# Performance work log

Hardware: AMD Instinct MI355X
Metric: run time of the kernel (lower is better)

The kernel has to match this reference:

```python
import jax, jax.numpy as jnp
import numpy as np

B, S, NC, ND, V = 16, 512, 10000, 10000, 128


def _rn(k, shape, scale=0.05):
    return jax.random.normal(k, shape, dtype=jnp.float32) * scale


def setup_inputs() -> dict:
    key = jax.random.key(0)
    ks = jax.random.split(key, 24)
    inp = {
        'c_seq': jax.random.randint(ks[0], (B, S), 0, NC),
        'd_seq': jax.random.randint(ks[1], (B, S), 0, ND),
        'r_seq': jax.random.uniform(ks[2], (B, S), dtype=jnp.float32),
        # embeddings / vectors
        'D1_w': _rn(ks[3], (ND, 1)),
        'D2_w': _rn(ks[4], (ND, V)),
        'v_r': _rn(ks[5], (V,)),
        'v_beta': _rn(ks[6], (V,)),
        # GRU (torch layout: gates ordered r,z,n; W_ih [3V,2V], W_hh [3V,V])
        'W_ih': _rn(ks[7], (3 * V, 2 * V)),
        'W_hh': _rn(ks[8], (3 * V, V)),
        'b_ih': jnp.zeros((3 * V,), jnp.float32),
        'b_hh': jnp.zeros((3 * V,), jnp.float32),
        # linear_1: V -> V -> V -> 1 (weights stored [in, out])
        'm1_W1': _rn(ks[9], (V, V)), 'm1_b1': jnp.zeros((V,), jnp.float32),
        'm1_W2': _rn(ks[10], (V, V)), 'm1_b2': jnp.zeros((V,), jnp.float32),
        'm1_W3': _rn(ks[11], (V, 1)), 'm1_b3': jnp.zeros((1,), jnp.float32),
        # linear_2: 3V -> V -> V -> 1
        'm2_W1': _rn(ks[12], (3 * V, V)), 'm2_b1': jnp.zeros((V,), jnp.float32),
        'm2_W2': _rn(ks[13], (V, V)), 'm2_b2': jnp.zeros((V,), jnp.float32),
        'm2_W3': _rn(ks[14], (V, 1)), 'm2_b3': jnp.zeros((1,), jnp.float32),
    }
    return inp


def _mlp(x, W1, b1, W2, b2, W3, b3):
    h = jax.nn.relu(x @ W1 + b1)
    h = jax.nn.relu(h @ W2 + b2)
    return h @ W3 + b3


def _gru_seq(x, W_ih, W_hh, b_ih, b_hh):
    # x: [B,S,2V] -> h_seq [B,S,V]; torch GRU gate order r,z,n
    xp = x @ W_ih.T + b_ih  # [B,S,3V]

    def step(h, xt):
        hp = h @ W_hh.T + b_hh
        xr, xz, xn = jnp.split(xt, 3, axis=-1)
        hr, hz, hn = jnp.split(hp, 3, axis=-1)
        r = jax.nn.sigmoid(xr + hr)
        z = jax.nn.sigmoid(xz + hz)
        n = jnp.tanh(xn + r * hn)
        h_new = (1.0 - z) * n + z * h
        return h_new, h_new

    h0 = jnp.zeros((x.shape[0], W_hh.shape[1]), x.dtype)
    _, hs = jax.lax.scan(step, h0, jnp.swapaxes(xp, 0, 1))  # [S,B,V]
    return jnp.swapaxes(hs, 0, 1)


def reference(c_seq, d_seq, r_seq, D1_w, D2_w, v_r, v_beta,
              W_ih, W_hh, b_ih, b_hh,
              m1_W1, m1_b1, m1_W2, m1_b2, m1_W3, m1_b3,
              m2_W1, m2_b1, m2_W2, m2_b2, m2_W3, m2_b3):
    v_d_seq = D2_w[d_seq]                     # [B,S,V]
    v_r_seq = r_seq[..., None] * v_r          # [B,S,V]

    h_seq = _gru_seq(jnp.concatenate([v_d_seq, v_r_seq], axis=-1),
                     W_ih, W_hh, b_ih, b_hh)  # [B,S,V]
    alpha_seq = _mlp(h_seq, m1_W1, m1_b1, m1_W2, m1_b2, m1_W3, m1_b3)[..., 0]  # [B,S]

    bidx = jnp.arange(c_seq.shape[0])

    def step(C, ins):
        c_t, vd_t, vr_t = ins                 # [B], [B,V], [B,V]
        beta_prev = C[bidx, c_t]              # gather: [B]
        v_beta_prev = beta_prev[:, None] * v_beta  # [B,V]
        new_c = _mlp(jnp.concatenate([v_beta_prev, vd_t, vr_t], axis=-1),
                     m2_W1, m2_b1, m2_W2, m2_b2, m2_W3, m2_b3)[:, 0]  # [B]
        C = C.at[bidx, c_t].set(new_c)        # scatter
        return C, (C, new_c)

    C0 = jnp.zeros((c_seq.shape[0], NC), jnp.float32)
    _, (C_seq, beta_seq) = jax.lax.scan(
        step, C0,
        (jnp.swapaxes(c_seq, 0, 1), jnp.swapaxes(v_d_seq, 0, 1), jnp.swapaxes(v_r_seq, 0, 1)))
    C_seq = jnp.swapaxes(C_seq, 0, 1)[..., None]   # [B,S,NC,1]
    beta_seq = jnp.swapaxes(beta_seq, 0, 1)        # [B,S]

    gamma_seq = D1_w[d_seq][..., 0]                # [B,S]
    return (alpha_seq, beta_seq, gamma_seq, h_seq, C_seq)
```

## Files before the change

### kernel.cpp

```cpp
#include <hip/hip_runtime.h>

#define Bq   16
#define Sq   512
#define Vq   128
#define NCq  10000

typedef __attribute__((ext_vector_type(8))) short short8v;
typedef __attribute__((ext_vector_type(4))) float f32x4;

#define OFF_XPF    0u
#define OFF_P1F    3145728u
#define OFF_WTIH   4194304u
#define OFF_WVRIH  4243456u
#define OFF_WVR1   4243840u
#define OFF_WVB    4243968u
#define OFF_W2T    4244096u
#define OFF_LIST   4260480u
#define OFF_CNT    4276864u

#define PLN 136
#define PLSZ (16*PLN+8)

__device__ __forceinline__ unsigned cvt_pk_bf16(float a, float b) {
    unsigned r;
    asm("v_cvt_pk_bf16_f32 %0, %1, %2" : "=v"(r) : "v"(a), "v"(b));
    return r;
}
__device__ __forceinline__ void barrier_lgkm() {
    asm volatile("s_waitcnt lgkmcnt(0)" ::: "memory");
    __builtin_amdgcn_sched_barrier(0);
    __builtin_amdgcn_s_barrier();
    __builtin_amdgcn_sched_barrier(0);
}
__device__ __forceinline__ void wait_vm4() {
    asm volatile("s_waitcnt vmcnt(4)" ::: "memory");
    __builtin_amdgcn_sched_barrier(0);
}
__device__ __forceinline__ void gload_lds16(const void* g, void* l) {
    __builtin_amdgcn_global_load_lds(
        (const __attribute__((address_space(1))) unsigned int*)g,
        (__attribute__((address_space(3))) unsigned int*)l, 16, 0, 0);
}

__global__ __launch_bounds__(256) void k0_prep(
    const int* __restrict__ c_seq, const int* __restrict__ d_seq,
    const float* __restrict__ D1_w,
    const float* __restrict__ W_ih,
    const float* __restrict__ v_r, const float* __restrict__ v_beta,
    const float* __restrict__ m2W1, const float* __restrict__ m2W2,
    float* __restrict__ ws, float* __restrict__ gamma_out)
{
    const int blk = blockIdx.x, tid = threadIdx.x;

    if (blk < 128) {
        float* WTIH = ws + OFF_WTIH;
        int base = blk * 384;
        for (int i = tid; i < 384; i += 256) {
            int e = base + i;
            int k = e / 384, g = e % 384;
            WTIH[e] = W_ih[g * 256 + k];
        }
    } else if (blk == 128) {
        float* WVRIH = ws + OFF_WVRIH;
        float* WVR1  = ws + OFF_WVR1;
        float* WVB   = ws + OFF_WVB;
        for (int g = tid; g < 384; g += 256) {
            float a = 0.f;
            for (int k = 0; k < 128; ++k) a = fmaf(v_r[k], W_ih[g * 256 + 128 + k], a);
            WVRIH[g] = a;
        }
        if (tid < 128) {
            float a = 0.f, b = 0.f;
            for (int k = 0; k < 128; ++k) {
                a = fmaf(v_r[k],    m2W1[(256 + k) * 128 + tid], a);
                b = fmaf(v_beta[k], m2W1[k * 128 + tid],         b);
            }
            WVR1[tid] = a; WVB[tid] = b;
        }
    } else if (blk < 145) {
        const int b = blk - 129;
        __shared__ int cs[Sq];
        __shared__ int po[Sq];
        for (int i = tid; i < Sq; i += 256) cs[i] = c_seq[b * Sq + i];
        __syncthreads();
        for (int t = tid; t < Sq; t += 256) {
            int c = cs[t];
            int p = -1;
            for (int u = t - 1; u >= 0; --u) if (cs[u] == c) { p = u; break; }
            po[t] = p;
        }
        __syncthreads();
        if (tid == 0) {
            int2* L = (int2*)(ws + OFF_LIST) + b * 512;
            int n = 0;
            for (int t = 0; t < Sq; ++t)
                if (po[t] >= 0) { L[n] = make_int2(t, po[t]); ++n; }
            ((int*)(ws + OFF_CNT))[b] = n;
        }
    } else if (blk < 161) {
        const int b = blk - 145;
        for (int s = tid; s < Sq; s += 256)
            gamma_out[b * Sq + s] = D1_w[d_seq[b * Sq + s]];
    } else {
        float* W2T = ws + OFF_W2T;
        for (int i = tid; i < 16384; i += 256) {
            int j = i >> 7, k = i & 127;
            W2T[i] = m2W2[k * 128 + j];
        }
    }
}

__global__ __launch_bounds__(256) void k1_gemm(
    const int* __restrict__ d_seq, const float* __restrict__ D2_w,
    const float* __restrict__ m2W1,
    const float* __restrict__ b_ih, const float* __restrict__ b_hh,
    const float* __restrict__ r_seq, const float* __restrict__ m2b1,
    float* __restrict__ ws)
{
    __shared__ float As[64 * 128];
    __shared__ float Bs[128 * 64];
    const int blk = blockIdx.x, tid = threadIdx.x;
    const int nc = blk & 7;
    const int m0 = (blk >> 3) * 64;
    const float* WTIH = ws + OFF_WTIH;

    const float4* D2v = (const float4*)D2_w;
    for (int e = tid; e < 2048; e += 256) {
        int r = e >> 5, q = e & 31;
        int d = d_seq[m0 + r];
        *(float4*)&As[r * 128 + 4 * q] = D2v[d * 32 + q];
    }
    for (int e = tid; e < 2048; e += 256) {
        int k = e >> 4, q = e & 15;
        float4 v;
        if (nc < 6) v = *(const float4*)&WTIH[k * 384 + nc * 64 + 4 * q];
        else        v = *(const float4*)&m2W1[(128 + k) * 128 + (nc - 6) * 64 + 4 * q];
        *(float4*)&Bs[k * 64 + 4 * q] = v;
    }
    __syncthreads();

    const int tx = tid & 15, ty = tid >> 4;
    const int c0 = 4 * tx, r0 = 4 * ty;
    float acc[4][4];
#pragma unroll
    for (int i = 0; i < 4; ++i)
#pragma unroll
        for (int j = 0; j < 4; ++j) acc[i][j] = 0.f;

    for (int k = 0; k < 128; ++k) {
        float4 bv = *(const float4*)&Bs[k * 64 + c0];
#pragma unroll
        for (int i = 0; i < 4; ++i) {
            float a = As[(r0 + i) * 128 + k];
            acc[i][0] = fmaf(a, bv.x, acc[i][0]);
            acc[i][1] = fmaf(a, bv.y, acc[i][1]);
            acc[i][2] = fmaf(a, bv.z, acc[i][2]);
            acc[i][3] = fmaf(a, bv.w, acc[i][3]);
        }
    }

    float rsv[4];
#pragma unroll
    for (int i = 0; i < 4; ++i) rsv[i] = r_seq[m0 + r0 + i];

    if (nc < 6) {
        const int grow0 = nc * 64 + c0;
        float4 bi  = *(const float4*)&b_ih[grow0];
        float4 wv4 = *(const float4*)&(ws + OFF_WVRIH)[grow0];
        float4 bh4 = make_float4(0.f, 0.f, 0.f, 0.f);
        if (nc < 4) bh4 = *(const float4*)&b_hh[grow0];
        float* XPF = ws + OFF_XPF;
        const int r4 = grow0 >> 2;
#pragma unroll
        for (int i = 0; i < 4; ++i) {
            int row = m0 + r0 + i;
            int t = row & 511, bb = row >> 9;
            float4 v;
            v.x = acc[i][0] + bi.x + bh4.x + rsv[i] * wv4.x;
            v.y = acc[i][1] + bi.y + bh4.y + rsv[i] * wv4.y;
            v.z = acc[i][2] + bi.z + bh4.z + rsv[i] * wv4.z;
            v.w = acc[i][3] + bi.w + bh4.w + rsv[i] * wv4.w;
            *(float4*)&XPF[((size_t)((bb >> 2) * 512 + t)) * 1536 + r4 * 16 + (bb & 3) * 4] = v;
        }
    } else {
        const int j0 = (nc - 6) * 64 + c0;
        float4 b1v = *(const float4*)&m2b1[j0];
        float4 wr1 = *(const float4*)&(ws + OFF_WVR1)[j0];
        float* P1F = ws + OFF_P1F;
#pragma unroll
        for (int i = 0; i < 4; ++i) {
            int row = m0 + r0 + i;
            int t = row & 511, bb = row >> 9;
            float4 v;
            v.x = acc[i][0] + b1v.x + rsv[i] * wr1.x;
            v.y = acc[i][1] + b1v.y + rsv[i] * wr1.y;
            v.z = acc[i][2] + b1v.z + rsv[i] * wr1.z;
            v.w = acc[i][3] + b1v.w + rsv[i] * wr1.w;
            *(float4*)&P1F[((size_t)(t * 16 + bb)) * 128 + j0] = v;
        }
    }
}

__global__ __launch_bounds__(512, 1) void k2_scan(
    const float* __restrict__ W_hh, const float* __restrict__ b_hh,
    const float* __restrict__ m2b2, const float* __restrict__ m2W3,
    const float* __restrict__ m2b3,
    float* __restrict__ ws,
    float* __restrict__ hseq_out, float* __restrict__ beta_out)
{
    __shared__ __align__(16) unsigned char smem[107040];
    const int tid = threadIdx.x;
    const int l = tid & 63, wv = tid >> 6;
    const int qq = l >> 4, cb = l & 15;
    const int bgid = blockIdx.x;

    if (bgid < 4) {
        unsigned short* hP  = (unsigned short*)smem;
        unsigned char*  xsl = smem + 8736;
        float* hstage = (float*)(smem + 8736 + 65536);
        const float* XPF = ws + OFF_XPF;

        short8v aH0[4], aH1[4], aH2[4];
#pragma unroll
        for (int kf = 0; kf < 4; ++kf) {
            const int kb = kf * 32 + qq * 8;
            const float* w0 = W_hh + (0 * 128 + 16 * wv + cb) * 128 + kb;
            const float* w1 = W_hh + (1 * 128 + 16 * wv + cb) * 128 + kb;
            const float* w2 = W_hh + (2 * 128 + 16 * wv + cb) * 128 + kb;
            short8v h0, h1, h2;
#pragma unroll
            for (int e = 0; e < 8; ++e) {
                unsigned u0 = __builtin_bit_cast(unsigned, w0[e]);
                unsigned u1 = __builtin_bit_cast(unsigned, w1[e]);
                unsigned u2 = __builtin_bit_cast(unsigned, w2[e]);
                h0[e] = (short)((u0 + 0x7fffu + ((u0 >> 16) & 1u)) >> 16);
                h1[e] = (short)((u1 + 0x7fffu + ((u1 >> 16) & 1u)) >> 16);
                h2[e] = (short)((u2 + 0x7fffu + ((u2 >> 16) & 1u)) >> 16);
            }
            aH0[kf] = h0; aH1[kf] = h1; aH2[kf] = h2;
        }
        f32x4 bhn4;
        {
            float4 t4 = *(const float4*)&b_hh[256 + 16 * wv + 4 * qq];
            bhn4[0] = t4.x; bhn4[1] = t4.y; bhn4[2] = t4.z; bhn4[3] = t4.w;
        }

        float hold[4] = {0.f, 0.f, 0.f, 0.f};
        for (int i = tid; i < 2 * PLSZ; i += 512) hP[i] = 0;
#pragma unroll
        for (int s = 0; s < 5; ++s)
            gload_lds16(XPF + ((size_t)(bgid * 512 + s)) * 1536 + tid * 4,
                        xsl + s * 8192 + tid * 16);
        __syncthreads();

        const float NL2E = -1.44269504f, L2E2 = 2.88539008f;
        for (int t = 0; t < 512; ++t) {
            if (t < 507)
                gload_lds16(XPF + ((size_t)(bgid * 512 + t + 5)) * 1536 + tid * 4,
                            xsl + ((t + 5) & 7) * 8192 + tid * 16);
            if ((t & 7) == 0 && t > 0) {
                const float* hb = hstage + (((t >> 3) + 1) & 1) * 4096;
#pragma unroll
                for (int r2 = 0; r2 < 2; ++r2) {
                    int e2 = tid * 2 + r2;
                    int ss = e2 >> 7, bq2 = (e2 >> 5) & 3, q = e2 & 31;
                    float4 v = *(const float4*)&hb[(ss * 4 + bq2) * 128 + q * 4];
                    *(float4*)&hseq_out[((size_t)((bgid * 4 + bq2) * 512 + (t - 8 + ss))) * 128 + q * 4] = v;
                }
            }

            const float* xc = (const float*)(xsl + (t & 7) * 8192) +
                              (4 * wv + qq) * 16 + (cb & 3) * 4;
            f32x4 px0 = *(const f32x4*)(xc);
            f32x4 px1 = *(const f32x4*)(xc + 512);
            f32x4 px2 = *(const f32x4*)(xc + 1024);

            const unsigned short* HI = hP + (t & 1) * PLSZ;
            unsigned short* HIn = hP + ((t + 1) & 1) * PLSZ;

            f32x4 C0a = px0, C1a = px1, C2a = bhn4;
            f32x4 C0b = {0.f,0.f,0.f,0.f}, C1b = {0.f,0.f,0.f,0.f}, C2b = {0.f,0.f,0.f,0.f};
            {
                short8v B0 = *(const short8v*)(HI + cb * PLN + 0 * 32 + qq * 8);
                short8v B1 = *(const short8v*)(HI + cb * PLN + 1 * 32 + qq * 8);
                short8v B2 = *(const short8v*)(HI + cb * PLN + 2 * 32 + qq * 8);
                short8v B3 = *(const short8v*)(HI + cb * PLN + 3 * 32 + qq * 8);
                C0a = __builtin_amdgcn_mfma_f32_16x16x32_bf16(aH0[0], B0, C0a, 0, 0, 0);
                C1a = __builtin_amdgcn_mfma_f32_16x16x32_bf16(aH1[0], B0, C1a, 0, 0, 0);
                C2a = __builtin_amdgcn_mfma_f32_16x16x32_bf16(aH2[0], B0, C2a, 0, 0, 0);
                C0b = __builtin_amdgcn_mfma_f32_16x16x32_bf16(aH0[1], B1, C0b, 0, 0, 0);
                C1b = __builtin_amdgcn_mfma_f32_16x16x32_bf16(aH1[1], B1, C1b, 0, 0, 0);
                C2b = __builtin_amdgcn_mfma_f32_16x16x32_bf16(aH2[1], B1, C2b, 0, 0, 0);
                C0a = __builtin_amdgcn_mfma_f32_16x16x32_bf16(aH0[2], B2, C0a, 0, 0, 0);
                C1a = __builtin_amdgcn_mfma_f32_16x16x32_bf16(aH1[2], B2, C1a, 0, 0, 0);
                C2a = __builtin_amdgcn_mfma_f32_16x16x32_bf16(aH2[2], B2, C2a, 0, 0, 0);
                C0b = __builtin_amdgcn_mfma_f32_16x16x32_bf16(aH0[3], B3, C0b, 0, 0, 0);
                C1b = __builtin_amdgcn_mfma_f32_16x16x32_bf16(aH1[3], B3, C1b, 0, 0, 0);
                C2b = __builtin_amdgcn_mfma_f32_16x16x32_bf16(aH2[3], B3, C2b, 0, 0, 0);
            }
            float hnew[4];
#pragma unroll
            for (int i = 0; i < 4; ++i) {
                float pr = C0a[i] + C0b[i];
                float pz = C1a[i] + C1b[i];
                float hn = C2a[i] + C2b[i];
                float r = __builtin_amdgcn_rcpf(1.f + __builtin_amdgcn_exp2f(pr * NL2E));
                float z = __builtin_amdgcn_rcpf(1.f + __builtin_amdgcn_exp2f(pz * NL2E));
                float npre = fmaf(r, hn, px2[i]);
                float n = fmaf(-2.f, __builtin_amdgcn_rcpf(1.f + __builtin_amdgcn_exp2f(npre * L2E2)), 1.f);
                float hv = fmaf(z, hold[i] - n, n);
                hold[i] = hv;
                hnew[i] = hv;
            }
            if (cb < 4) {
                float* hst = hstage + ((t >> 3) & 1) * 4096;
                *(float4*)&hst[((t & 7) * 4 + cb) * 128 + 16 * wv + 4 * qq] =
                    make_float4(hnew[0], hnew[1], hnew[2], hnew[3]);
                uint2 hw;
                hw.x = cvt_pk_bf16(hnew[0], hnew[1]);
                hw.y = cvt_pk_bf16(hnew[2], hnew[3]);
                *(uint2*)(HIn + cb * PLN + 16 * wv + 4 * qq) = hw;
            }
            wait_vm4();
            barrier_lgkm();
        }
#pragma unroll
        for (int r2 = 0; r2 < 2; ++r2) {
            int e2 = tid * 2 + r2;
            int ss = e2 >> 7, bq2 = (e2 >> 5) & 3, q = e2 & 31;
            float4 v = *(const float4*)&hstage[4096 + (ss * 4 + bq2) * 128 + q * 4];
            *(float4*)&hseq_out[((size_t)((bgid * 4 + bq2) * 512 + (504 + ss))) * 128 + q * 4] = v;
        }
    } else {
        const int d = bgid - 4;
        float* h1L = (float*)smem;
        const float* P1F = ws + OFF_P1F;
        const float* W2T = ws + OFF_W2T;

        const float* src = P1F + (size_t)d * 4096;
        for (int i = tid; i < 1024; i += 512) {
            float4 v = *(const float4*)&src[i * 4];
            v.x = fmaxf(v.x, 0.f); v.y = fmaxf(v.y, 0.f);
            v.z = fmaxf(v.z, 0.f); v.w = fmaxf(v.w, 0.f);
            *(float4*)&h1L[i * 4] = v;
        }
        __syncthreads();

        const int r = tid >> 4, jg = tid & 15;
        float acc[8];
#pragma unroll
        for (int jj = 0; jj < 8; ++jj) acc[jj] = m2b2[jg * 8 + jj];
        for (int k4 = 0; k4 < 32; ++k4) {
            float4 h4 = *(const float4*)&h1L[r * 128 + k4 * 4];
#pragma unroll
            for (int jj = 0; jj < 8; ++jj) {
                float4 w4 = *(const float4*)&W2T[(jg * 8 + jj) * 128 + k4 * 4];
                acc[jj] = fmaf(h4.x, w4.x, acc[jj]);
                acc[jj] = fmaf(h4.y, w4.y, acc[jj]);
                acc[jj] = fmaf(h4.z, w4.z, acc[jj]);
                acc[jj] = fmaf(h4.w, w4.w, acc[jj]);
            }
        }
        float part = 0.f;
#pragma unroll
        for (int jj = 0; jj < 8; ++jj)
            part = fmaf(fmaxf(acc[jj], 0.f), m2W3[jg * 8 + jj], part);
        part += __shfl_xor(part, 1);
        part += __shfl_xor(part, 2);
        part += __shfl_xor(part, 4);
        part += __shfl_xor(part, 8);
        if (jg == 0) {
            int R = d * 32 + r;
            beta_out[(R & 15) * 512 + (R >> 4)] = part + m2b3[0];
        }
    }
}

__global__ __launch_bounds__(64, 1) void k2c_fix(
    const float* __restrict__ m2b2, const float* __restrict__ m2W3,
    const float* __restrict__ m2b3,
    float* __restrict__ ws, float* __restrict__ beta_out)
{
    __shared__ __align__(16) float W2L[128 * 129];
    __shared__ float betaF[512];
    __shared__ __align__(16) float h1L[128];
    const int b = blockIdx.x, l = threadIdx.x;
    const float* W2T = ws + OFF_W2T;
    const float* P1F = ws + OFF_P1F;

    for (int i = l; i < 16384; i += 64) {
        int j = i >> 7, k = i & 127;
        W2L[j * 129 + k] = W2T[i];
    }
    for (int i = l; i < 512; i += 64) betaF[i] = beta_out[b * 512 + i];

    const float2 wvb2 = *(const float2*)&(ws + OFF_WVB)[2 * l];
    const float2 b22  = *(const float2*)&m2b2[2 * l];
    const float2 w32  = *(const float2*)&m2W3[2 * l];
    const float b3v = m2b3[0];
    const int n = ((const int*)(ws + OFF_CNT))[b];
    const int2* L = (const int2*)(ws + OFF_LIST) + b * 512;
    barrier_lgkm();

    for (int i = 0; i < n; ++i) {
        int2 tp = L[i];
        float bp = betaF[tp.y];
        float2 p1 = *(const float2*)&P1F[((size_t)(tp.x * 16 + b)) * 128 + 2 * l];
        float h0 = fmaxf(0.f, fmaf(bp, wvb2.x, p1.x));
        float h1 = fmaxf(0.f, fmaf(bp, wvb2.y, p1.y));
        *(float2*)&h1L[2 * l] = make_float2(h0, h1);
        barrier_lgkm();
        float a0 = b22.x, a1 = b22.y;
        const float* w0 = &W2L[(2 * l) * 129];
        const float* w1 = &W2L[(2 * l + 1) * 129];
        for (int k4 = 0; k4 < 32; ++k4) {
            float4 h4 = *(const float4*)&h1L[k4 * 4];
            float4 u0 = *(const float4*)&w0[k4 * 4];
            float4 u1 = *(const float4*)&w1[k4 * 4];
            a0 = fmaf(h4.x, u0.x, a0); a0 = fmaf(h4.y, u0.y, a0);
            a0 = fmaf(h4.z, u0.z, a0); a0 = fmaf(h4.w, u0.w, a0);
            a1 = fmaf(h4.x, u1.x, a1); a1 = fmaf(h4.y, u1.y, a1);
            a1 = fmaf(h4.z, u1.z, a1); a1 = fmaf(h4.w, u1.w, a1);
        }
        float part = fmaf(fmaxf(a0, 0.f), w32.x, fmaxf(a1, 0.f) * w32.y);
#pragma unroll
        for (int off = 1; off < 64; off <<= 1) part += __shfl_xor(part, off);
        float bta = part + b3v;
        if (l == 0) {
            betaF[tp.x] = bta;
            beta_out[b * 512 + tp.x] = bta;
        }
        barrier_lgkm();
    }
}

__global__ __launch_bounds__(256) void k2b_fill(
    const int* __restrict__ c_seq, const float* __restrict__ beta_in,
    float* __restrict__ C_out)
{
    __shared__ int   scs[Sq];
    __shared__ float sbt[Sq];
    const int bid = blockIdx.x, tid = threadIdx.x;
    const int b = bid / 40, rem = bid % 40;
    const int chunk = rem >> 2, q = rem & 3;

    for (int i = tid; i < Sq; i += 256) {
        scs[i] = c_seq[b * Sq + i];
        sbt[i] = beta_in[b * Sq + i];
    }
    __syncthreads();

    const int c0 = chunk * 1024 + tid * 4;
    if (c0 >= NCq) return;

    float cur0 = 0.f, cur1 = 0.f, cur2 = 0.f, cur3 = 0.f;
    const int tlo = q * 128, thi = tlo + 128;
    float* base = C_out + (size_t)b * Sq * NCq + c0;

    for (int t = 0; t < tlo; ++t) {
        int ct = scs[t] - c0; float bv = sbt[t];
        cur0 = (ct == 0) ? bv : cur0;
        cur1 = (ct == 1) ? bv : cur1;
        cur2 = (ct == 2) ? bv : cur2;
        cur3 = (ct == 3) ? bv : cur3;
    }
    for (int t = tlo; t < thi; ++t) {
        int ct = scs[t] - c0; float bv = sbt[t];
        cur0 = (ct == 0) ? bv : cur0;
        cur1 = (ct == 1) ? bv : cur1;
        cur2 = (ct == 2) ? bv : cur2;
        cur3 = (ct == 3) ? bv : cur3;
        *(float4*)(base + (size_t)t * NCq) = make_float4(cur0, cur1, cur2, cur3);
    }
}

__global__ __launch_bounds__(256) void k3_alpha(
    const float* __restrict__ hseq,
    const float* __restrict__ W1, const float* __restrict__ b1,
    const float* __restrict__ W2, const float* __restrict__ b2,
    const float* __restrict__ W3, const float* __restrict__ b3,
    float* __restrict__ alpha_out)
{
    __shared__ float Hs[32 * 128];
    __shared__ float T1[32 * 128];
    __shared__ float red[4][16];
    const int blk = blockIdx.x, tid = threadIdx.x;
    const int row0 = blk * 32;

    for (int e = tid; e < 1024; e += 256) {
        int r = e >> 5, q = e & 31;
        *(float4*)&Hs[r * 128 + 4 * q] =
            *(const float4*)&hseq[(size_t)(row0 + r) * 128 + 4 * q];
    }
    __syncthreads();

    const int j = tid & 127, rh = tid >> 7;
    const float b1j = b1[j], b2j = b2[j], w3j = W3[j];
    float acc[16];
#pragma unroll
    for (int r = 0; r < 16; ++r) acc[r] = b1j;
    for (int k = 0; k < 128; ++k) {
        float w = W1[k * 128 + j];
#pragma unroll
        for (int r = 0; r < 16; ++r)
            acc[r] = fmaf(Hs[(rh * 16 + r) * 128 + k], w, acc[r]);
    }
#pragma unroll
    for (int r = 0; r < 16; ++r) {
        acc[r] = fmaxf(acc[r], 0.f);
        T1[(rh * 16 + r) * 128 + j] = acc[r];
    }
    __syncthreads();
    float acc2[16];
#pragma unroll
    for (int r = 0; r < 16; ++r) acc2[r] = b2j;
    for (int k = 0; k < 128; ++k) {
        float w = W2[k * 128 + j];
#pragma unroll
        for (int r = 0; r < 16; ++r)
            acc2[r] = fmaf(T1[(rh * 16 + r) * 128 + k], w, acc2[r]);
    }
#pragma unroll
    for (int r = 0; r < 16; ++r) {
        float p = fmaxf(acc2[r], 0.f) * w3j;
#pragma unroll
        for (int off = 1; off < 64; off <<= 1) p += __shfl_xor(p, off);
        if ((tid & 63) == 0) red[tid >> 6][r] = p;
    }
    __syncthreads();
    if (tid < 32) {
        int rr = tid & 15, g = tid >> 4;
        alpha_out[row0 + g * 16 + rr] = red[2 * g][rr] + red[2 * g + 1][rr] + b3[0];
    }
}

extern "C" void kernel_launch(void* const* d_in, const int* in_sizes, int n_in,
                              void* d_out, int out_size, void* d_ws, size_t ws_size,
                              hipStream_t stream) {
    const int*   c_seq = (const int*)d_in[0];
    const int*   d_seq = (const int*)d_in[1];
    const float* r_seq = (const float*)d_in[2];
    const float* D1_w  = (const float*)d_in[3];
    const float* D2_w  = (const float*)d_in[4];
    const float* v_r   = (const float*)d_in[5];
    const float* v_b   = (const float*)d_in[6];
    const float* W_ih  = (const float*)d_in[7];
    const float* W_hh  = (const float*)d_in[8];
    const float* b_ih  = (const float*)d_in[9];
    const float* b_hh  = (const float*)d_in[10];
    const float* m1W1  = (const float*)d_in[11];
    const float* m1b1  = (const float*)d_in[12];
    const float* m1W2  = (const float*)d_in[13];
    const float* m1b2  = (const float*)d_in[14];
    const float* m1W3  = (const float*)d_in[15];
    const float* m1b3  = (const float*)d_in[16];
    const float* m2W1  = (const float*)d_in[17];
    const float* m2b1  = (const float*)d_in[18];
    const float* m2W2  = (const float*)d_in[19];
    const float* m2b2  = (const float*)d_in[20];
    const float* m2W3  = (const float*)d_in[21];
    const float* m2b3  = (const float*)d_in[22];

    float* out   = (float*)d_out;
    float* alpha = out;
    float* beta  = out + 8192;
    float* gamma = out + 16384;
    float* hseq  = out + 24576;
    float* Cseq  = out + 1073152;
    float* ws    = (float*)d_ws;

    hipLaunchKernelGGL(k0_prep, dim3(162), dim3(256), 0, stream,
                       c_seq, d_seq, D1_w, W_ih, v_r, v_b, m2W1, m2W2, ws, gamma);
    hipLaunchKernelGGL(k1_gemm, dim3(1024), dim3(256), 0, stream,
                       d_seq, D2_w, m2W1, b_ih, b_hh, r_seq, m2b1, ws);
    hipLaunchKernelGGL(k2_scan, dim3(260), dim3(512), 0, stream,
                       W_hh, b_hh, m2b2, m2W3, m2b3, ws, hseq, beta);
    hipLaunchKernelGGL(k2c_fix, dim3(16), dim3(64), 0, stream,
                       m2b2, m2W3, m2b3, ws, beta);
    hipLaunchKernelGGL(k2b_fill, dim3(640), dim3(256), 0, stream,
                       c_seq, beta, Cseq);
    hipLaunchKernelGGL(k3_alpha, dim3(256), dim3(256), 0, stream,
                       hseq, m1W1, m1b1, m1W2, m1b2, m1W3, m1b3, alpha);
}
```

Measured before the change: 668.8 us.

## Halve GRU scan block size with two row-groups per wave, rework fix kernel

The recurrent GRU scan now runs with 256 threads per block, and each wave handles two 16-row gate groups. The weight fragments and accumulators are doubled per wave, and the MFMA chain is interleaved across the two sub-groups sharing each B fragment. The aim is to cut barrier participants and expose more independent MFMAs per wave on the serial critical path. The XP slot layout changes to 6144-byte slots loaded with two LDS copies per thread. The non-scan blocks now handle half as many rows each, doubling their grid, and the fix kernel is rewritten with 128 active threads doing one output each. The cost is higher register pressure from the 24 resident weight fragments, and the slot layout change must match the producer kernel.

```diff
diff --git a/kernel.cpp b/kernel.cpp
--- a/kernel.cpp
+++ b/kernel.cpp
@@ -20,6 +20,8 @@
 
 #define PLN 136
 #define PLSZ (16*PLN+8)
+#define SLOTB 6144
+#define LSLOT 8192
 
 __device__ __forceinline__ unsigned cvt_pk_bf16(float a, float b) {
     unsigned r;
@@ -32,8 +34,8 @@
     __builtin_amdgcn_s_barrier();
     __builtin_amdgcn_sched_barrier(0);
 }
-__device__ __forceinline__ void wait_vm4() {
-    asm volatile("s_waitcnt vmcnt(4)" ::: "memory");
+__device__ __forceinline__ void wait_vm8() {
+    asm volatile("s_waitcnt vmcnt(8)" ::: "memory");
     __builtin_amdgcn_sched_barrier(0);
 }
 __device__ __forceinline__ void gload_lds16(const void* g, void* l) {
@@ -201,7 +203,7 @@
     }
 }
 
-__global__ __launch_bounds__(512, 1) void k2_scan(
+__global__ __launch_bounds__(256, 1) void k2_scan(
     const float* __restrict__ W_hh, const float* __restrict__ b_hh,
     const float* __restrict__ m2b2, const float* __restrict__ m2W3,
     const float* __restrict__ m2b3,
@@ -219,115 +221,131 @@
         unsigned char*  xsl = smem + 8736;
         float* hstage = (float*)(smem + 8736 + 65536);
         const float* XPF = ws + OFF_XPF;
-
-        short8v aH0[4], aH1[4], aH2[4];
-#pragma unroll
-        for (int kf = 0; kf < 4; ++kf) {
-            const int kb = kf * 32 + qq * 8;
-            const float* w0 = W_hh + (0 * 128 + 16 * wv + cb) * 128 + kb;
-            const float* w1 = W_hh + (1 * 128 + 16 * wv + cb) * 128 + kb;
-            const float* w2 = W_hh + (2 * 128 + 16 * wv + cb) * 128 + kb;
-            short8v h0, h1, h2;
-#pragma unroll
-            for (int e = 0; e < 8; ++e) {
-                unsigned u0 = __builtin_bit_cast(unsigned, w0[e]);
-                unsigned u1 = __builtin_bit_cast(unsigned, w1[e]);
-                unsigned u2 = __builtin_bit_cast(unsigned, w2[e]);
-                h0[e] = (short)((u0 + 0x7fffu + ((u0 >> 16) & 1u)) >> 16);
-                h1[e] = (short)((u1 + 0x7fffu + ((u1 >> 16) & 1u)) >> 16);
-                h2[e] = (short)((u2 + 0x7fffu + ((u2 >> 16) & 1u)) >> 16);
-            }
-            aH0[kf] = h0; aH1[kf] = h1; aH2[kf] = h2;
-        }
-        f32x4 bhn4;
-        {
-            float4 t4 = *(const float4*)&b_hh[256 + 16 * wv + 4 * qq];
-            bhn4[0] = t4.x; bhn4[1] = t4.y; bhn4[2] = t4.z; bhn4[3] = t4.w;
-        }
-
-        float hold[4] = {0.f, 0.f, 0.f, 0.f};
-        for (int i = tid; i < 2 * PLSZ; i += 512) hP[i] = 0;
-#pragma unroll
-        for (int s = 0; s < 5; ++s)
-            gload_lds16(XPF + ((size_t)(bgid * 512 + s)) * 1536 + tid * 4,
-                        xsl + s * 8192 + tid * 16);
+        const unsigned char* XPB = (const unsigned char*)XPF;
+
+        short8v aH[2][3][4];
+#pragma unroll
+        for (int sub = 0; sub < 2; ++sub) {
+            const int rg = 2 * wv + sub;
+#pragma unroll
+            for (int g = 0; g < 3; ++g) {
+                const float* wrow = W_hh + (g * 128 + 16 * rg + cb) * 128;
+#pragma unroll
+                for (int kf = 0; kf < 4; ++kf) {
+                    short8v h;
+#pragma unroll
+                    for (int e = 0; e < 8; ++e) {
+                        unsigned u = __builtin_bit_cast(unsigned, wrow[kf * 32 + qq * 8 + e]);
+                        h[e] = (short)((u + 0x7fffu + ((u >> 16) & 1u)) >> 16);
+                    }
+                    aH[sub][g][kf] = h;
+                }
+            }
+        }
+        f32x4 bhn4[2];
+#pragma unroll
+        for (int sub = 0; sub < 2; ++sub) {
+            float4 t4 = *(const float4*)&b_hh[256 + 16 * (2 * wv + sub) + 4 * qq];
+            bhn4[sub][0] = t4.x; bhn4[sub][1] = t4.y; bhn4[sub][2] = t4.z; bhn4[sub][3] = t4.w;
+        }
+
+        float hold[2][4];
+#pragma unroll
+        for (int sub = 0; sub < 2; ++sub)
+#pragma unroll
+            for (int i = 0; i < 4; ++i) hold[sub][i] = 0.f;
+
+        for (int i = tid; i < 2 * PLSZ; i += 256) hP[i] = 0;
+#pragma unroll
+        for (int s = 0; s < 5; ++s) {
+            const unsigned char* gsrc = XPB + ((size_t)(bgid * 512 + s)) * SLOTB;
+            gload_lds16(gsrc + tid * 16, xsl + s * LSLOT + tid * 16);
+            gload_lds16(gsrc + 4096 + tid * 16, xsl + s * LSLOT + 4096 + tid * 16);
+        }
         __syncthreads();
 
         const float NL2E = -1.44269504f, L2E2 = 2.88539008f;
         for (int t = 0; t < 512; ++t) {
-            if (t < 507)
-                gload_lds16(XPF + ((size_t)(bgid * 512 + t + 5)) * 1536 + tid * 4,
-                            xsl + ((t + 5) & 7) * 8192 + tid * 16);
+            if (t < 507) {
+                const unsigned char* gsrc = XPB + ((size_t)(bgid * 512 + t + 5)) * SLOTB;
+                unsigned char* dst = xsl + ((t + 5) & 7) * LSLOT;
+                gload_lds16(gsrc + tid * 16, dst + tid * 16);
+                gload_lds16(gsrc + 4096 + tid * 16, dst + 4096 + tid * 16);
+            }
             if ((t & 7) == 0 && t > 0) {
                 const float* hb = hstage + (((t >> 3) + 1) & 1) * 4096;
 #pragma unroll
-                for (int r2 = 0; r2 < 2; ++r2) {
-                    int e2 = tid * 2 + r2;
-                    int ss = e2 >> 7, bq2 = (e2 >> 5) & 3, q = e2 & 31;
+                for (int r2 = 0; r2 < 4; ++r2) {
+                    int e2 = tid * 4 + r2;
+                    int ss = e2 >> 7, rem = e2 & 127;
+                    int bq2 = rem >> 5, q = rem & 31;
                     float4 v = *(const float4*)&hb[(ss * 4 + bq2) * 128 + q * 4];
                     *(float4*)&hseq_out[((size_t)((bgid * 4 + bq2) * 512 + (t - 8 + ss))) * 128 + q * 4] = v;
                 }
             }
 
-            const float* xc = (const float*)(xsl + (t & 7) * 8192) +
-                              (4 * wv + qq) * 16 + (cb & 3) * 4;
-            f32x4 px0 = *(const f32x4*)(xc);
-            f32x4 px1 = *(const f32x4*)(xc + 512);
-            f32x4 px2 = *(const f32x4*)(xc + 1024);
-
+            const float* xc = (const float*)(xsl + (t & 7) * LSLOT) + (cb & 3) * 4;
             const unsigned short* HI = hP + (t & 1) * PLSZ;
             unsigned short* HIn = hP + ((t + 1) & 1) * PLSZ;
 
-            f32x4 C0a = px0, C1a = px1, C2a = bhn4;
-            f32x4 C0b = {0.f,0.f,0.f,0.f}, C1b = {0.f,0.f,0.f,0.f}, C2b = {0.f,0.f,0.f,0.f};
-            {
-                short8v B0 = *(const short8v*)(HI + cb * PLN + 0 * 32 + qq * 8);
-                short8v B1 = *(const short8v*)(HI + cb * PLN + 1 * 32 + qq * 8);
-                short8v B2 = *(const short8v*)(HI + cb * PLN + 2 * 32 + qq * 8);
-                short8v B3 = *(const short8v*)(HI + cb * PLN + 3 * 32 + qq * 8);
-                C0a = __builtin_amdgcn_mfma_f32_16x16x32_bf16(aH0[0], B0, C0a, 0, 0, 0);
-                C1a = __builtin_amdgcn_mfma_f32_16x16x32_bf16(aH1[0], B0, C1a, 0, 0, 0);
-                C2a = __builtin_amdgcn_mfma_f32_16x16x32_bf16(aH2[0], B0, C2a, 0, 0, 0);
-                C0b = __builtin_amdgcn_mfma_f32_16x16x32_bf16(aH0[1], B1, C0b, 0, 0, 0);
-                C1b = __builtin_amdgcn_mfma_f32_16x16x32_bf16(aH1[1], B1, C1b, 0, 0, 0);
-                C2b = __builtin_amdgcn_mfma_f32_16x16x32_bf16(aH2[1], B1, C2b, 0, 0, 0);
-                C0a = __builtin_amdgcn_mfma_f32_16x16x32_bf16(aH0[2], B2, C0a, 0, 0, 0);
-                C1a = __builtin_amdgcn_mfma_f32_16x16x32_bf16(aH1[2], B2, C1a, 0, 0, 0);
-                C2a = __builtin_amdgcn_mfma_f32_16x16x32_bf16(aH2[2], B2, C2a, 0, 0, 0);
-                C0b = __builtin_amdgcn_mfma_f32_16x16x32_bf16(aH0[3], B3, C0b, 0, 0, 0);
-                C1b = __builtin_amdgcn_mfma_f32_16x16x32_bf16(aH1[3], B3, C1b, 0, 0, 0);
-                C2b = __builtin_amdgcn_mfma_f32_16x16x32_bf16(aH2[3], B3, C2b, 0, 0, 0);
-            }
-            float hnew[4];
-#pragma unroll
-            for (int i = 0; i < 4; ++i) {
-                float pr = C0a[i] + C0b[i];
-                float pz = C1a[i] + C1b[i];
-                float hn = C2a[i] + C2b[i];
-                float r = __builtin_amdgcn_rcpf(1.f + __builtin_amdgcn_exp2f(pr * NL2E));
-                float z = __builtin_amdgcn_rcpf(1.f + __builtin_amdgcn_exp2f(pz * NL2E));
-                float npre = fmaf(r, hn, px2[i]);
-                float n = fmaf(-2.f, __builtin_amdgcn_rcpf(1.f + __builtin_amdgcn_exp2f(npre * L2E2)), 1.f);
-                float hv = fmaf(z, hold[i] - n, n);
-                hold[i] = hv;
-                hnew[i] = hv;
+            f32x4 px2s[2];
+            f32x4 C[2][3];
+#pragma unroll
+            for (int sub = 0; sub < 2; ++sub) {
+                const int rg = 2 * wv + sub;
+                C[sub][0] = *(const f32x4*)(xc + (0 * 32 + rg * 4 + qq) * 16);
+                C[sub][1] = *(const f32x4*)(xc + (1 * 32 + rg * 4 + qq) * 16);
+                px2s[sub] = *(const f32x4*)(xc + (2 * 32 + rg * 4 + qq) * 16);
+                C[sub][2] = bhn4[sub];
+            }
+#pragma unroll
+            for (int kf = 0; kf < 4; ++kf) {
+                short8v B = *(const short8v*)(HI + cb * PLN + kf * 32 + qq * 8);
+#pragma unroll
+                for (int sub = 0; sub < 2; ++sub) {
+                    C[sub][0] = __builtin_amdgcn_mfma_f32_16x16x32_bf16(aH[sub][0][kf], B, C[sub][0], 0, 0, 0);
+                    C[sub][1] = __builtin_amdgcn_mfma_f32_16x16x32_bf16(aH[sub][1][kf], B, C[sub][1], 0, 0, 0);
+                    C[sub][2] = __builtin_amdgcn_mfma_f32_16x16x32_bf16(aH[sub][2][kf], B, C[sub][2], 0, 0, 0);
+                }
+            }
+            float hnew[2][4];
+#pragma unroll
+            for (int sub = 0; sub < 2; ++sub) {
+#pragma unroll
+                for (int i = 0; i < 4; ++i) {
+                    float pr = C[sub][0][i];
+                    float pz = C[sub][1][i];
+                    float hn = C[sub][2][i];
+                    float r = __builtin_amdgcn_rcpf(1.f + __builtin_amdgcn_exp2f(pr * NL2E));
+                    float z = __builtin_amdgcn_rcpf(1.f + __builtin_amdgcn_exp2f(pz * NL2E));
+                    float npre = fmaf(r, hn, px2s[sub][i]);
+                    float n = fmaf(-2.f, __builtin_amdgcn_rcpf(1.f + __builtin_amdgcn_exp2f(npre * L2E2)), 1.f);
+                    float hv = fmaf(z, hold[sub][i] - n, n);
+                    hold[sub][i] = hv;
+                    hnew[sub][i] = hv;
+                }
             }
             if (cb < 4) {
                 float* hst = hstage + ((t >> 3) & 1) * 4096;
-                *(float4*)&hst[((t & 7) * 4 + cb) * 128 + 16 * wv + 4 * qq] =
-                    make_float4(hnew[0], hnew[1], hnew[2], hnew[3]);
-                uint2 hw;
-                hw.x = cvt_pk_bf16(hnew[0], hnew[1]);
-                hw.y = cvt_pk_bf16(hnew[2], hnew[3]);
-                *(uint2*)(HIn + cb * PLN + 16 * wv + 4 * qq) = hw;
-            }
-            wait_vm4();
+#pragma unroll
+                for (int sub = 0; sub < 2; ++sub) {
+                    const int rg = 2 * wv + sub;
+                    *(float4*)&hst[((t & 7) * 4 + cb) * 128 + 16 * rg + 4 * qq] =
+                        make_float4(hnew[sub][0], hnew[sub][1], hnew[sub][2], hnew[sub][3]);
+                    uint2 hw;
+                    hw.x = cvt_pk_bf16(hnew[sub][0], hnew[sub][1]);
+                    hw.y = cvt_pk_bf16(hnew[sub][2], hnew[sub][3]);
+                    *(uint2*)(HIn + cb * PLN + 16 * rg + 4 * qq) = hw;
+                }
+            }
+            wait_vm8();
             barrier_lgkm();
         }
 #pragma unroll
-        for (int r2 = 0; r2 < 2; ++r2) {
-            int e2 = tid * 2 + r2;
-            int ss = e2 >> 7, bq2 = (e2 >> 5) & 3, q = e2 & 31;
+        for (int r2 = 0; r2 < 4; ++r2) {
+            int e2 = tid * 4 + r2;
+            int ss = e2 >> 7, rem = e2 & 127;
+            int bq2 = rem >> 5, q = rem & 31;
             float4 v = *(const float4*)&hstage[4096 + (ss * 4 + bq2) * 128 + q * 4];
             *(float4*)&hseq_out[((size_t)((bgid * 4 + bq2) * 512 + (504 + ss))) * 128 + q * 4] = v;
         }
@@ -337,8 +355,8 @@
         const float* P1F = ws + OFF_P1F;
         const float* W2T = ws + OFF_W2T;
 
-        const float* src = P1F + (size_t)d * 4096;
-        for (int i = tid; i < 1024; i += 512) {
+        const float* src = P1F + (size_t)d * 2048;
+        for (int i = tid; i < 512; i += 256) {
             float4 v = *(const float4*)&src[i * 4];
             v.x = fmaxf(v.x, 0.f); v.y = fmaxf(v.y, 0.f);
             v.z = fmaxf(v.z, 0.f); v.w = fmaxf(v.w, 0.f);
@@ -370,63 +388,63 @@
         part += __shfl_xor(part, 4);
         part += __shfl_xor(part, 8);
         if (jg == 0) {
-            int R = d * 32 + r;
+            int R = d * 16 + r;
             beta_out[(R & 15) * 512 + (R >> 4)] = part + m2b3[0];
         }
     }
 }
 
-__global__ __launch_bounds__(64, 1) void k2c_fix(
+__global__ __launch_bounds__(256, 1) void k2c_fix(
     const float* __restrict__ m2b2, const float* __restrict__ m2W3,
     const float* __restrict__ m2b3,
     float* __restrict__ ws, float* __restrict__ beta_out)
 {
-    __shared__ __align__(16) float W2L[128 * 129];
+    __shared__ float W2L[128 * 129];
     __shared__ float betaF[512];
-    __shared__ __align__(16) float h1L[128];
-    const int b = blockIdx.x, l = threadIdx.x;
+    __shared__ float h1L[128];
+    __shared__ float red2[2];
+    const int b = blockIdx.x, tid = threadIdx.x;
     const float* W2T = ws + OFF_W2T;
     const float* P1F = ws + OFF_P1F;
 
-    for (int i = l; i < 16384; i += 64) {
+    for (int i = tid; i < 16384; i += 256) {
         int j = i >> 7, k = i & 127;
         W2L[j * 129 + k] = W2T[i];
     }
-    for (int i = l; i < 512; i += 64) betaF[i] = beta_out[b * 512 + i];
-
-    const float2 wvb2 = *(const float2*)&(ws + OFF_WVB)[2 * l];
-    const float2 b22  = *(const float2*)&m2b2[2 * l];
-    const float2 w32  = *(const float2*)&m2W3[2 * l];
+    for (int i = tid; i < 512; i += 256) betaF[i] = beta_out[b * 512 + i];
+
+    const bool pa = tid < 128;
+    float wvbj = 0.f, b2j = 0.f, w3j = 0.f;
+    if (pa) {
+        wvbj = (ws + OFF_WVB)[tid];
+        b2j  = m2b2[tid];
+        w3j  = m2W3[tid];
+    }
     const float b3v = m2b3[0];
     const int n = ((const int*)(ws + OFF_CNT))[b];
     const int2* L = (const int2*)(ws + OFF_LIST) + b * 512;
-    barrier_lgkm();
+    __syncthreads();
 
     for (int i = 0; i < n; ++i) {
         int2 tp = L[i];
-        float bp = betaF[tp.y];
-        float2 p1 = *(const float2*)&P1F[((size_t)(tp.x * 16 + b)) * 128 + 2 * l];
-        float h0 = fmaxf(0.f, fmaf(bp, wvb2.x, p1.x));
-        float h1 = fmaxf(0.f, fmaf(bp, wvb2.y, p1.y));
-        *(float2*)&h1L[2 * l] = make_float2(h0, h1);
+        if (pa) {
+            float bp = betaF[tp.y];
+            float p1 = P1F[((size_t)(tp.x * 16 + b)) * 128 + tid];
+            h1L[tid] = fmaxf(0.f, fmaf(bp, wvbj, p1));
+        }
         barrier_lgkm();
-        float a0 = b22.x, a1 = b22.y;
-        const float* w0 = &W2L[(2 * l) * 129];
-        const float* w1 = &W2L[(2 * l + 1) * 129];
-        for (int k4 = 0; k4 < 32; ++k4) {
-            float4 h4 = *(const float4*)&h1L[k4 * 4];
-            float4 u0 = *(const float4*)&w0[k4 * 4];
-            float4 u1 = *(const float4*)&w1[k4 * 4];
-            a0 = fmaf(h4.x, u0.x, a0); a0 = fmaf(h4.y, u0.y, a0);
-            a0 = fmaf(h4.z, u0.z, a0); a0 = fmaf(h4.w, u0.w, a0);
-            a1 = fmaf(h4.x, u1.x, a1); a1 = fmaf(h4.y, u1.y, a1);
-            a1 = fmaf(h4.z, u1.z, a1); a1 = fmaf(h4.w, u1.w, a1);
-        }
-        float part = fmaf(fmaxf(a0, 0.f), w32.x, fmaxf(a1, 0.f) * w32.y);
-#pragma unroll
-        for (int off = 1; off < 64; off <<= 1) part += __shfl_xor(part, off);
-        float bta = part + b3v;
-        if (l == 0) {
+        if (pa) {
+            float a = b2j;
+            const float* wr = &W2L[tid * 129];
+            for (int k = 0; k < 128; ++k) a = fmaf(wr[k], h1L[k], a);
+            float part = fmaxf(a, 0.f) * w3j;
+#pragma unroll
+            for (int off = 1; off < 64; off <<= 1) part += __shfl_xor(part, off);
+            if ((tid & 63) == 0) red2[tid >> 6] = part;
+        }
+        barrier_lgkm();
+        if (tid == 0) {
+            float bta = red2[0] + red2[1] + b3v;
             betaF[tp.x] = bta;
             beta_out[b * 512 + tp.x] = bta;
         }
@@ -573,9 +591,9 @@
                        c_seq, d_seq, D1_w, W_ih, v_r, v_b, m2W1, m2W2, ws, gamma);
     hipLaunchKernelGGL(k1_gemm, dim3(1024), dim3(256), 0, stream,
                        d_seq, D2_w, m2W1, b_ih, b_hh, r_seq, m2b1, ws);
-    hipLaunchKernelGGL(k2_scan, dim3(260), dim3(512), 0, stream,
+    hipLaunchKernelGGL(k2_scan, dim3(516), dim3(256), 0, stream,
                        W_hh, b_hh, m2b2, m2W3, m2b3, ws, hseq, beta);
-    hipLaunchKernelGGL(k2c_fix, dim3(16), dim3(64), 0, stream,
+    hipLaunchKernelGGL(k2c_fix, dim3(16), dim3(256), 0, stream,
                        m2b2, m2W3, m2b3, ws, beta);
     hipLaunchKernelGGL(k2b_fill, dim3(640), dim3(256), 0, stream,
                        c_seq, beta, Cseq);
```

New measurement: 699.4 us. +4.6%, slower.
